# Kernel optimization log

Hardware: AMD Instinct MI355X
Metric: run time of the kernel (lower is better)

The kernel has to match this reference:

```python
import jax, jax.numpy as jnp
import numpy as np

DT = 0.05        # Euler step size
S_EULER = 2      # Euler steps between consecutive events, and after the last one (prop_to_end)


def setup_inputs() -> dict:
    key = jax.random.key(0)
    B, H, D, K, E = 512, 512, 128, 64, 256
    ks = jax.random.split(key, 16)

    def w(k, fan_in, fan_out):
        return jax.random.normal(k, (fan_in, fan_out), jnp.float32) / np.float32(np.sqrt(fan_in))

    X = jax.random.normal(ks[0], (K, E, D), jnp.float32)
    M = jax.random.bernoulli(ks[1], 0.5, (K, E, D)).astype(jnp.float32)
    # unique sample indices per event (irregular observation pattern, no scatter collisions)
    batch_idx = jax.vmap(lambda k: jax.random.permutation(k, B)[:E])(jax.random.split(ks[2], K))
    sample_idx = jnp.arange(B)
    b = lambda n: jnp.full((n,), 0.01, jnp.float32)  # torch init: bias filled with 0.01
    return {
        'X': X, 'M': M, 'batch_idx': batch_idx, 'sample_idx': sample_idx,
        'Wi': w(ks[3], D + H, H), 'bi': b(H),
        'Wf': w(ks[4], D + H, H), 'bf': b(H),
        'Wo': w(ks[5], D + H, H), 'bo': b(H),
        'Wc': w(ks[6], D + H, H), 'bc': b(H),
        'W1': w(ks[7], H, H), 'b1': b(H),
        'W2': w(ks[8], H, H), 'b2': b(H),
        'Wp1': w(ks[9], H, H), 'bp1': b(H),
        'Wp2': w(ks[10], H, D), 'bp2': b(D),
    }


def reference(X, M, batch_idx, sample_idx,
              Wi, bi, Wf, bf, Wo, bo, Wc, bc,
              W1, b1, W2, b2, Wp1, bp1, Wp2, bp2):
    B = sample_idx.shape[0]
    H = W1.shape[0]
    h0 = jnp.zeros((B, H), X.dtype)
    c0 = jnp.zeros((B, H), X.dtype)

    def euler(h):  # h <- h + dt * ODEFunc(h)
        return h + DT * (jnp.tanh(h @ W1 + b1) @ W2 + b2)

    def p_model(h):  # Linear -> ReLU -> (Dropout p=0, eval) -> Linear
        return jax.nn.relu(h @ Wp1 + bp1) @ Wp2 + bp2

    def step(carry, xs):
        h, c, loss, tot_m = carry
        Xo, Mo, idx = xs  # [E,D], [E,D], [E]
        for _ in range(S_EULER):
            h = euler(h)
        p = p_model(h)
        loss = loss + jnp.sum(jnp.abs(Xo - p[idx]) * Mo)
        tot_m = tot_m + jnp.sum(Mo)
        inp = jnp.concatenate([Xo, h[idx]], axis=-1)  # [E, D+H]
        ig = jax.nn.sigmoid(inp @ Wi + bi)
        fg = jax.nn.sigmoid(inp @ Wf + bf)
        og = jax.nn.sigmoid(inp @ Wo + bo)
        ct = jnp.tanh(inp @ Wc + bc)
        c_new = fg * c[idx] + ig * ct
        h_new = og * jnp.tanh(c_new)
        return (h.at[idx].set(h_new), c.at[idx].set(c_new), loss, tot_m), None

    init = (h0, c0, jnp.float32(0.0), jnp.float32(0.0))
    (h, c, loss, tot_m), _ = jax.lax.scan(step, init, (X, M, batch_idx))
    for _ in range(S_EULER):  # prop_to_end up to T
        h = euler(h)
    return jnp.stack([loss, loss / tot_m])
```

## Files before the change

### kernel.cpp

```cpp
#include <hip/hip_runtime.h>
#include <hip/hip_fp16.h>
#include <stdint.h>

#define Kn 64
#define En 256
#define Bn 512
#define Hn 512
#define Dn 128
#define NBLK 256
#define NTH  256
#define DT_C 0.05f


typedef _Float16 f16x8 __attribute__((ext_vector_type(8)));
typedef float    f32x4 __attribute__((ext_vector_type(4)));
typedef unsigned long long u64;

__device__ __forceinline__ float sigm(float x){ return 1.0f/(1.0f + __expf(-x)); }

__device__ __forceinline__ u64 ald(const u64* p){
  return __hip_atomic_load(p, __ATOMIC_RELAXED, __HIP_MEMORY_SCOPE_AGENT);
}
__device__ __forceinline__ void ast(u64* p, u64 v){
  __hip_atomic_store(p, v, __ATOMIC_RELAXED, __HIP_MEMORY_SCOPE_AGENT);
}

union HU { __half h[8]; u64 q[2]; uint32_t w[4]; };

__global__ void k_init(int* __restrict__ pos, float* __restrict__ acc,
                       int* __restrict__ ctr, uint32_t* __restrict__ hf){
  int i = blockIdx.x*blockDim.x + threadIdx.x;
  if (i < Kn*Bn) pos[i] = -1;
  if (i < 2) acc[i] = 0.0f;
  if (i < 1024) ctr[i] = 0;
  if (i < Hn*Hn/2) hf[i] = 0;
}

__global__ void k_scatter(const int* __restrict__ bidx, int* __restrict__ pos){
  int i = blockIdx.x*blockDim.x + threadIdx.x;
  if (i < Kn*En){
    int k = i >> 8;
    int e = i & (En-1);
    pos[(k << 9) | bidx[i]] = e;
  }
}

__global__ void k_cvt_frag(const float* __restrict__ src, __half* __restrict__ dst,
                           int KT, int N, int n){
  int i = blockIdx.x*blockDim.x + threadIdx.x;
  if (i >= n) return;
  int C = i / (KT*512);
  int r = i % (KT*512);
  int T = r >> 9;
  int q = r & 511;
  int l = q >> 3, e = q & 7;
  int srow = T*32 + ((l>>4)<<3) + e;
  int scol = C*16 + (l&15);
  dst[i] = __float2half(src[(size_t)srow*N + scol]);
}

__device__ __forceinline__ void gsync(int* c, int tgt){
  asm volatile("s_waitcnt vmcnt(0)" ::: "memory");
  __syncthreads();
  if (threadIdx.x == 0){
    __hip_atomic_fetch_add(c, 1, __ATOMIC_RELAXED, __HIP_MEMORY_SCOPE_AGENT);
    while (__hip_atomic_load(c, __ATOMIC_RELAXED, __HIP_MEMORY_SCOPE_AGENT) < tgt)
      __builtin_amdgcn_s_sleep(1);
  }
  __syncthreads();
}

__global__ __launch_bounds__(NTH, 1) void k_main(
  const float* __restrict__ X, const float* __restrict__ Mm,
  const int* __restrict__ pos, const __half* __restrict__ WF,
  __half* __restrict__ Hf, __half* __restrict__ Tf,
  const float* __restrict__ bi_, const float* __restrict__ bf_,
  const float* __restrict__ bo_, const float* __restrict__ bc_,
  const float* __restrict__ b1_, const float* __restrict__ b2_,
  const float* __restrict__ bp1_, const float* __restrict__ bp2_,
  float* __restrict__ acc, int* __restrict__ ctrbase)
{
  const __half* W1F  = WF;
  const __half* W2F  = WF + 262144;
  const __half* Wp1F = WF + 524288;
  const __half* Wp2F = WF + 786432;
  const __half* WgF  = WF + 851968;

  const int t    = threadIdx.x;
  const int bid  = blockIdx.x;
  const int s    = bid & 7;
  const int g    = bid >> 3;
  const int w    = t >> 6;
  const int lane = t & 63;

  int* ctr = ctrbase + g*32;

  __shared__ __align__(16) __half Afrag[16*512];
  __shared__ __align__(16) __half Xfrag[4*512];
  __shared__ __align__(16) float  outb[20*256];
  __shared__ float redbuf[8];

  const int row = t >> 4;
  const int q4  = t & 15;
  const int sc  = s*64 + q4*4;
  float Hreg[4] = {0,0,0,0};
  float Creg[4] = {0,0,0,0};
  float vb1[4], vb2[4], vbp1[4], vbi[4], vbf[4], vbo[4], vbc[4];
  #pragma unroll
  for (int i=0;i<4;i++){
    vb1[i]=b1_[sc+i]; vb2[i]=b2_[sc+i]; vbp1[i]=bp1_[sc+i];
    vbi[i]=bi_[sc+i]; vbf[i]=bf_[sc+i]; vbo[i]=bo_[sc+i]; vbc[i]=bc_[sc+i];
  }
  const float vbp2 = bp2_[s*16 + q4];

  f16x8 W1r[16], W2r[16], Wp1r[16];
  {
    const size_t cb = (size_t)(s*4 + w)*16*512 + lane*8;
    #pragma unroll
    for (int kt=0; kt<16; kt++){
      W1r[kt]  = *(const f16x8*)(W1F  + cb + kt*512);
      W2r[kt]  = *(const f16x8*)(W2F  + cb + kt*512);
      Wp1r[kt] = *(const f16x8*)(Wp1F + cb + kt*512);
    }
  }

  float loss_loc = 0.f, m_loc = 0.f;
  int round = 0;
  const int grow = g*16 + row;

  for (int k=0; k<Kn; k++){
    const int epos = pos[(k<<9) + grow];

    #pragma unroll 1
    for (int ph=0; ph<4; ph++){
      const __half* src = (ph & 1) ? Tf : Hf;
      {
        const int ar = t & 15, ch = t >> 4;
        const u64* sp = (const u64*)(src + ((size_t)(g*16+ar))*512 + ch*32);
        u64 v[8];
        #pragma unroll
        for (int i=0;i<8;i++) v[i] = ald(sp+i);
        #pragma unroll
        for (int kg=0;kg<4;kg++){
          u64* d = (u64*)(Afrag + ch*512 + (ar + 16*kg)*8);
          d[0] = v[2*kg]; d[1] = v[2*kg+1];
        }
      }
      __syncthreads();
      {
        f32x4 a4 = {0,0,0,0};
        if (!(ph & 1)){
          #pragma unroll
          for (int kt=0; kt<16; kt++){
            f16x8 a = *(const f16x8*)(Afrag + kt*512 + lane*8);
            a4 = __builtin_amdgcn_mfma_f32_16x16x32_f16(a, W1r[kt], a4, 0,0,0);
          }
        } else {
          #pragma unroll
          for (int kt=0; kt<16; kt++){
            f16x8 a = *(const f16x8*)(Afrag + kt*512 + lane*8);
            a4 = __builtin_amdgcn_mfma_f32_16x16x32_f16(a, W2r[kt], a4, 0,0,0);
          }
        }
        float* o = outb + w*256 + ((lane>>4)*4)*16 + (lane&15);
        o[0]=a4[0]; o[16]=a4[1]; o[32]=a4[2]; o[48]=a4[3];
      }
      __syncthreads();
      {
        const float* o = outb + (q4>>2)*256 + row*16 + (q4&3)*4;
        float v0=o[0], v1=o[1], v2=o[2], v3=o[3];
        HU u;
        if (!(ph & 1)){
          u.h[0]=__float2half(tanhf(v0+vb1[0])); u.h[1]=__float2half(tanhf(v1+vb1[1]));
          u.h[2]=__float2half(tanhf(v2+vb1[2])); u.h[3]=__float2half(tanhf(v3+vb1[3]));
          ast((u64*)(Tf + (size_t)grow*512 + sc), u.q[0]);
        } else {
          Hreg[0] += DT_C*(v0+vb2[0]); Hreg[1] += DT_C*(v1+vb2[1]);
          Hreg[2] += DT_C*(v2+vb2[2]); Hreg[3] += DT_C*(v3+vb2[3]);
          u.h[0]=__float2half(Hreg[0]); u.h[1]=__float2half(Hreg[1]);
          u.h[2]=__float2half(Hreg[2]); u.h[3]=__float2half(Hreg[3]);
          ast((u64*)(Hf + (size_t)grow*512 + sc), u.q[0]);
        }
      }
      gsync(ctr, 8*(++round));
    }

    {
      {
        const int ar = t & 15, ch = t >> 4;
        const u64* sp = (const u64*)(Hf + ((size_t)(g*16+ar))*512 + ch*32);
        u64 v[8];
        #pragma unroll
        for (int i=0;i<8;i++) v[i] = ald(sp+i);
        #pragma unroll
        for (int kg=0;kg<4;kg++){
          u64* d = (u64*)(Afrag + ch*512 + (ar + 16*kg)*8);
          d[0] = v[2*kg]; d[1] = v[2*kg+1];
        }
      }
      if (t < 64){
        const int ar = t & 15, ch = t >> 4;
        const int e = pos[(k<<9) + g*16 + ar];
        float xv[32];
        if (e >= 0){
          const float4* xp = (const float4*)(X + ((size_t)(k*En+e))*Dn + ch*32);
          #pragma unroll
          for (int i=0;i<8;i++){
            float4 f = xp[i];
            xv[4*i]=f.x; xv[4*i+1]=f.y; xv[4*i+2]=f.z; xv[4*i+3]=f.w;
          }
        } else {
          #pragma unroll
          for (int i=0;i<32;i++) xv[i]=0.f;
        }
        #pragma unroll
        for (int kg=0;kg<4;kg++){
          HU u;
          #pragma unroll
          for (int e8=0;e8<8;e8++) u.h[e8] = __float2half(xv[kg*8+e8]);
          u64* d = (u64*)(Xfrag + ch*512 + (ar + 16*kg)*8);
          d[0] = u.q[0]; d[1] = u.q[1];
        }
      }
      __syncthreads();
      {
        f32x4 a4 = {0,0,0,0};
        #pragma unroll
        for (int kt=0; kt<16; kt++){
          f16x8 a = *(const f16x8*)(Afrag + kt*512 + lane*8);
          a4 = __builtin_amdgcn_mfma_f32_16x16x32_f16(a, Wp1r[kt], a4, 0,0,0);
        }
        float* o = outb + (16+w)*256 + ((lane>>4)*4)*16 + (lane&15);
        o[0]=a4[0]; o[16]=a4[1]; o[32]=a4[2]; o[48]=a4[3];
      }
      #pragma unroll 1
      for (int i=0;i<4;i++){
        const int Cg = w*32 + s*4 + i;
        const __half* wb = WgF + (size_t)Cg*20*512;
        f32x4 a4 = {0,0,0,0};
        #pragma unroll 4
        for (int kt=0; kt<4; kt++){
          f16x8 a = *(const f16x8*)(Xfrag + kt*512 + lane*8);
          f16x8 b = *(const f16x8*)(wb + kt*512 + lane*8);
          a4 = __builtin_amdgcn_mfma_f32_16x16x32_f16(a, b, a4, 0,0,0);
        }
        #pragma unroll 4
        for (int kt=4; kt<20; kt++){
          f16x8 a = *(const f16x8*)(Afrag + (kt-4)*512 + lane*8);
          f16x8 b = *(const f16x8*)(wb + kt*512 + lane*8);
          a4 = __builtin_amdgcn_mfma_f32_16x16x32_f16(a, b, a4, 0,0,0);
        }
        float* o = outb + (w*4+i)*256 + ((lane>>4)*4)*16 + (lane&15);
        o[0]=a4[0]; o[16]=a4[1]; o[32]=a4[2]; o[48]=a4[3];
      }
      __syncthreads();
      {
        const float* o = outb + (16+(q4>>2))*256 + row*16 + (q4&3)*4;
        HU u;
        u.h[0]=__float2half(fmaxf(o[0]+vbp1[0],0.f));
        u.h[1]=__float2half(fmaxf(o[1]+vbp1[1],0.f));
        u.h[2]=__float2half(fmaxf(o[2]+vbp1[2],0.f));
        u.h[3]=__float2half(fmaxf(o[3]+vbp1[3],0.f));
        ast((u64*)(Tf + (size_t)grow*512 + sc), u.q[0]);
      }
      gsync(ctr, 8*(++round));
    }

    {
      {
        const int ar = t & 15, ch = t >> 4;
        const u64* sp = (const u64*)(Tf + ((size_t)(g*16+ar))*512 + ch*32);
        u64 v[8];
        #pragma unroll
        for (int i=0;i<8;i++) v[i] = ald(sp+i);
        #pragma unroll
        for (int kg=0;kg<4;kg++){
          u64* d = (u64*)(Afrag + ch*512 + (ar + 16*kg)*8);
          d[0] = v[2*kg]; d[1] = v[2*kg+1];
        }
      }
      __syncthreads();
      {
        const __half* wb = Wp2F + (size_t)s*16*512;
        f32x4 a4 = {0,0,0,0};
        #pragma unroll
        for (int kt2=0; kt2<4; kt2++){
          const int kt = w*4 + kt2;
          f16x8 a = *(const f16x8*)(Afrag + kt*512 + lane*8);
          f16x8 b = *(const f16x8*)(wb + kt*512 + lane*8);
          a4 = __builtin_amdgcn_mfma_f32_16x16x32_f16(a, b, a4, 0,0,0);
        }
        float* o = outb + (16+w)*256 + ((lane>>4)*4)*16 + (lane&15);
        o[0]=a4[0]; o[16]=a4[1]; o[32]=a4[2]; o[48]=a4[3];
      }
      if (epos >= 0){
        const int sub = q4 >> 2, off = row*16 + (q4&3)*4;
        const float4 pi = *(const float4*)(outb + (0*4+sub)*256 + off);
        const float4 pf = *(const float4*)(outb + (1*4+sub)*256 + off);
        const float4 po = *(const float4*)(outb + (2*4+sub)*256 + off);
        const float4 pc = *(const float4*)(outb + (3*4+sub)*256 + off);
        HU hu;
        const float gi[4]={pi.x,pi.y,pi.z,pi.w}, gf[4]={pf.x,pf.y,pf.z,pf.w};
        const float go[4]={po.x,po.y,po.z,po.w}, gc[4]={pc.x,pc.y,pc.z,pc.w};
        #pragma unroll
        for (int i=0;i<4;i++){
          float ig = sigm(gi[i] + vbi[i]);
          float fg = sigm(gf[i] + vbf[i]);
          float og = sigm(go[i] + vbo[i]);
          float ct = tanhf(gc[i] + vbc[i]);
          Creg[i] = fg*Creg[i] + ig*ct;
          Hreg[i] = og*tanhf(Creg[i]);
          hu.h[i] = __float2half(Hreg[i]);
        }
        ast((u64*)(Hf + (size_t)grow*512 + sc), hu.q[0]);
      }
      __syncthreads();
      if (epos >= 0){
        float p = outb[16*256 + row*16+q4] + outb[17*256 + row*16+q4]
                + outb[18*256 + row*16+q4] + outb[19*256 + row*16+q4] + vbp2;
        const int d = s*16 + q4;
        float xo = X[((size_t)(k*En+epos))*Dn + d];
        float mo = Mm[((size_t)(k*En+epos))*Dn + d];
        loss_loc += fabsf(xo - p)*mo;
        m_loc    += mo;
      }
      gsync(ctr, 8*(++round));
    }
  }

  #pragma unroll
  for (int off=32; off>0; off>>=1){
    loss_loc += __shfl_down(loss_loc, off);
    m_loc    += __shfl_down(m_loc, off);
  }
  if (lane == 0){ redbuf[w] = loss_loc; redbuf[4+w] = m_loc; }
  __syncthreads();
  if (t == 0){
    atomicAdd(acc+0, redbuf[0]+redbuf[1]+redbuf[2]+redbuf[3]);
    atomicAdd(acc+1, redbuf[4]+redbuf[5]+redbuf[6]+redbuf[7]);
  }
}

__global__ void k_fin(const float* __restrict__ acc, float* __restrict__ out){
  if (threadIdx.x == 0){
    out[0] = acc[0];
    out[1] = acc[0]/acc[1];
  }
}

extern "C" void kernel_launch(void* const* d_in, const int* in_sizes, int n_in,
                              void* d_out, int out_size, void* d_ws, size_t ws_size,
                              hipStream_t stream)
{
  const float* X   = (const float*)d_in[0];
  const float* Mm  = (const float*)d_in[1];
  const int*  bidx = (const int*)d_in[2];
  const float* Wi  = (const float*)d_in[4];
  const float* bi  = (const float*)d_in[5];
  const float* Wf  = (const float*)d_in[6];
  const float* bff = (const float*)d_in[7];
  const float* Wo  = (const float*)d_in[8];
  const float* bo  = (const float*)d_in[9];
  const float* Wc  = (const float*)d_in[10];
  const float* bc  = (const float*)d_in[11];
  const float* W1  = (const float*)d_in[12];
  const float* b1  = (const float*)d_in[13];
  const float* W2  = (const float*)d_in[14];
  const float* b2  = (const float*)d_in[15];
  const float* Wp1 = (const float*)d_in[16];
  const float* bp1 = (const float*)d_in[17];
  const float* Wp2 = (const float*)d_in[18];
  const float* bp2 = (const float*)d_in[19];

  char* ws = (char*)d_ws;
  int*    pos = (int*)ws;
  float*  acc = (float*)(ws + 131072);
  int*    ctr = (int*)(ws + 131200);
  __half* Hf  = (__half*)(ws + 1048576);
  __half* Tf  = (__half*)(ws + 1572864);
  __half* WF  = (__half*)(ws + 4194304);

  k_init   <<<512, 256, 0, stream>>>(pos, acc, ctr, (uint32_t*)Hf);
  k_scatter<<<(Kn*En + 255)/256, 256, 0, stream>>>(bidx, pos);

  k_cvt_frag<<<(262144+255)/256, 256, 0, stream>>>(W1,  WF,          16, 512, 262144);
  k_cvt_frag<<<(262144+255)/256, 256, 0, stream>>>(W2,  WF + 262144, 16, 512, 262144);
  k_cvt_frag<<<(262144+255)/256, 256, 0, stream>>>(Wp1, WF + 524288, 16, 512, 262144);
  k_cvt_frag<<<(65536 +255)/256, 256, 0, stream>>>(Wp2, WF + 786432, 16, 128, 65536);
  k_cvt_frag<<<(327680+255)/256, 256, 0, stream>>>(Wi,  WF + 851968,            20, 512, 327680);
  k_cvt_frag<<<(327680+255)/256, 256, 0, stream>>>(Wf,  WF + 851968 + 327680,   20, 512, 327680);
  k_cvt_frag<<<(327680+255)/256, 256, 0, stream>>>(Wo,  WF + 851968 + 655360,   20, 512, 327680);
  k_cvt_frag<<<(327680+255)/256, 256, 0, stream>>>(Wc,  WF + 851968 + 983040,   20, 512, 327680);

  k_main<<<NBLK, NTH, 0, stream>>>(X, Mm, pos, WF, Hf, Tf,
                                   bi, bff, bo, bc, b1, b2, bp1, bp2, acc, ctr);
  k_fin<<<1, 64, 0, stream>>>(acc, (float*)d_out);
}
```

Baseline: 1.916 ms.

## Replace counter barrier with per-block flags and defer Wp2 stage into next event

The shared atomic-counter group barrier becomes per-block round flags: each block publishes its own flag and polls the eight flags of its group, so the fetch-add read-modify-write is gone. The Wp2 projection and loss computation for event k are moved into the first Euler phase of event k+1, using separate buffers (T2f for the ReLU hidden state, Hf2 for the LSTM-updated h), which removes one grid-group sync per event. This cuts the syncs per event from six to five, at the cost of extra buffers, a selection between Hf and Hf2 per row, and an epilogue that handles the last event.

```diff
diff --git a/kernel.cpp b/kernel.cpp
--- a/kernel.cpp
+++ b/kernel.cpp
@@ -25,14 +25,14 @@
   __hip_atomic_store(p, v, __ATOMIC_RELAXED, __HIP_MEMORY_SCOPE_AGENT);
 }
 
-union HU { __half h[8]; u64 q[2]; uint32_t w[4]; };
+union HU { __half h[8]; u64 q[2]; };
 
 __global__ void k_init(int* __restrict__ pos, float* __restrict__ acc,
-                       int* __restrict__ ctr, uint32_t* __restrict__ hf){
+                       int* __restrict__ flg, uint32_t* __restrict__ hf){
   int i = blockIdx.x*blockDim.x + threadIdx.x;
   if (i < Kn*Bn) pos[i] = -1;
   if (i < 2) acc[i] = 0.0f;
-  if (i < 1024) ctr[i] = 0;
+  if (i < 32*8*32) flg[i] = 0;
   if (i < Hn*Hn/2) hf[i] = 0;
 }
 
@@ -59,26 +59,26 @@
   dst[i] = __float2half(src[(size_t)srow*N + scol]);
 }
 
-__device__ __forceinline__ void gsync(int* c, int tgt){
-  asm volatile("s_waitcnt vmcnt(0)" ::: "memory");
-  __syncthreads();
-  if (threadIdx.x == 0){
-    __hip_atomic_fetch_add(c, 1, __ATOMIC_RELAXED, __HIP_MEMORY_SCOPE_AGENT);
-    while (__hip_atomic_load(c, __ATOMIC_RELAXED, __HIP_MEMORY_SCOPE_AGENT) < tgt)
-      __builtin_amdgcn_s_sleep(1);
-  }
-  __syncthreads();
+__device__ __forceinline__ f32x4 mv16(const __half* Af, const f16x8* Wr, int lane){
+  f32x4 a = {0.f,0.f,0.f,0.f};
+  #pragma unroll
+  for (int kt=0; kt<16; kt++){
+    f16x8 av = *(const f16x8*)(Af + kt*512 + lane*8);
+    a = __builtin_amdgcn_mfma_f32_16x16x32_f16(av, Wr[kt], a, 0,0,0);
+  }
+  return a;
 }
 
 __global__ __launch_bounds__(NTH, 1) void k_main(
   const float* __restrict__ X, const float* __restrict__ Mm,
   const int* __restrict__ pos, const __half* __restrict__ WF,
   __half* __restrict__ Hf, __half* __restrict__ Tf,
+  __half* __restrict__ T2f, __half* __restrict__ Hf2,
   const float* __restrict__ bi_, const float* __restrict__ bf_,
   const float* __restrict__ bo_, const float* __restrict__ bc_,
   const float* __restrict__ b1_, const float* __restrict__ b2_,
   const float* __restrict__ bp1_, const float* __restrict__ bp2_,
-  float* __restrict__ acc, int* __restrict__ ctrbase)
+  float* __restrict__ acc, int* __restrict__ flg)
 {
   const __half* W1F  = WF;
   const __half* W2F  = WF + 262144;
@@ -92,10 +92,10 @@
   const int g    = bid >> 3;
   const int w    = t >> 6;
   const int lane = t & 63;
-
-  int* ctr = ctrbase + g*32;
+  int* flgbase = flg + g*8*32;
 
   __shared__ __align__(16) __half Afrag[16*512];
+  __shared__ __align__(16) __half Bfrag[16*512];
   __shared__ __align__(16) __half Xfrag[4*512];
   __shared__ __align__(16) float  outb[20*256];
   __shared__ float redbuf[8];
@@ -115,7 +115,7 @@
 
   f16x8 W1r[16], W2r[16], Wp1r[16];
   {
-    const size_t cb = (size_t)(s*4 + w)*16*512 + lane*8;
+    const size_t cb = (size_t)(s*4 + w)*16*512 + (size_t)lane*8;
     #pragma unroll
     for (int kt=0; kt<16; kt++){
       W1r[kt]  = *(const f16x8*)(W1F  + cb + kt*512);
@@ -125,206 +125,268 @@
   }
 
   float loss_loc = 0.f, m_loc = 0.f;
-  int round = 0;
+  int rnd = 0;
   const int grow = g*16 + row;
+
+#define POLL() do{                                                         \
+    if (t < 8){                                                            \
+      while (__hip_atomic_load(flgbase + t*32, __ATOMIC_RELAXED,           \
+                               __HIP_MEMORY_SCOPE_AGENT) < rnd)            \
+        __builtin_amdgcn_s_sleep(1);                                       \
+    }                                                                      \
+    __syncthreads();                                                       \
+  }while(0)
+
+#define PUBLISH() do{                                                      \
+    asm volatile("s_waitcnt vmcnt(0)" ::: "memory");                       \
+    __syncthreads();                                                       \
+    rnd++;                                                                 \
+    if (t == 0)                                                            \
+      __hip_atomic_store(flgbase + s*32, rnd, __ATOMIC_RELAXED,            \
+                         __HIP_MEMORY_SCOPE_AGENT);                        \
+  }while(0)
+
+#define STAGE(DST, SRCPTR) do{                                             \
+    const int ar = t & 15, ch = t >> 4;                                    \
+    const u64* sp = (const u64*)((SRCPTR) + ((size_t)(g*16+ar))*512 + ch*32); \
+    u64 v[8];                                                              \
+    _Pragma("unroll") for (int i=0;i<8;i++) v[i] = ald(sp+i);              \
+    _Pragma("unroll")                                                      \
+    for (int kg=0;kg<4;kg++){                                              \
+      u64* d = (u64*)((DST) + ch*512 + (ar + 16*kg)*8);                    \
+      d[0] = v[2*kg]; d[1] = v[2*kg+1];                                    \
+    }                                                                      \
+  }while(0)
 
   for (int k=0; k<Kn; k++){
     const int epos = pos[(k<<9) + grow];
 
-    #pragma unroll 1
-    for (int ph=0; ph<4; ph++){
-      const __half* src = (ph & 1) ? Tf : Hf;
-      {
-        const int ar = t & 15, ch = t >> 4;
-        const u64* sp = (const u64*)(src + ((size_t)(g*16+ar))*512 + ch*32);
-        u64 v[8];
-        #pragma unroll
-        for (int i=0;i<8;i++) v[i] = ald(sp+i);
-        #pragma unroll
-        for (int kg=0;kg<4;kg++){
-          u64* d = (u64*)(Afrag + ch*512 + (ar + 16*kg)*8);
-          d[0] = v[2*kg]; d[1] = v[2*kg+1];
-        }
-      }
-      __syncthreads();
-      {
-        f32x4 a4 = {0,0,0,0};
-        if (!(ph & 1)){
-          #pragma unroll
-          for (int kt=0; kt<16; kt++){
-            f16x8 a = *(const f16x8*)(Afrag + kt*512 + lane*8);
-            a4 = __builtin_amdgcn_mfma_f32_16x16x32_f16(a, W1r[kt], a4, 0,0,0);
-          }
-        } else {
-          #pragma unroll
-          for (int kt=0; kt<16; kt++){
-            f16x8 a = *(const f16x8*)(Afrag + kt*512 + lane*8);
-            a4 = __builtin_amdgcn_mfma_f32_16x16x32_f16(a, W2r[kt], a4, 0,0,0);
-          }
-        }
-        float* o = outb + w*256 + ((lane>>4)*4)*16 + (lane&15);
-        o[0]=a4[0]; o[16]=a4[1]; o[32]=a4[2]; o[48]=a4[3];
-      }
-      __syncthreads();
-      {
-        const float* o = outb + (q4>>2)*256 + row*16 + (q4&3)*4;
-        float v0=o[0], v1=o[1], v2=o[2], v3=o[3];
-        HU u;
-        if (!(ph & 1)){
-          u.h[0]=__float2half(tanhf(v0+vb1[0])); u.h[1]=__float2half(tanhf(v1+vb1[1]));
-          u.h[2]=__float2half(tanhf(v2+vb1[2])); u.h[3]=__float2half(tanhf(v3+vb1[3]));
-          ast((u64*)(Tf + (size_t)grow*512 + sc), u.q[0]);
-        } else {
-          Hreg[0] += DT_C*(v0+vb2[0]); Hreg[1] += DT_C*(v1+vb2[1]);
-          Hreg[2] += DT_C*(v2+vb2[2]); Hreg[3] += DT_C*(v3+vb2[3]);
-          u.h[0]=__float2half(Hreg[0]); u.h[1]=__float2half(Hreg[1]);
-          u.h[2]=__float2half(Hreg[2]); u.h[3]=__float2half(Hreg[3]);
-          ast((u64*)(Hf + (size_t)grow*512 + sc), u.q[0]);
-        }
-      }
-      gsync(ctr, 8*(++round));
-    }
-
-    {
-      {
-        const int ar = t & 15, ch = t >> 4;
-        const u64* sp = (const u64*)(Hf + ((size_t)(g*16+ar))*512 + ch*32);
-        u64 v[8];
-        #pragma unroll
-        for (int i=0;i<8;i++) v[i] = ald(sp+i);
-        #pragma unroll
-        for (int kg=0;kg<4;kg++){
-          u64* d = (u64*)(Afrag + ch*512 + (ar + 16*kg)*8);
-          d[0] = v[2*kg]; d[1] = v[2*kg+1];
-        }
-      }
-      if (t < 64){
-        const int ar = t & 15, ch = t >> 4;
-        const int e = pos[(k<<9) + g*16 + ar];
-        float xv[32];
-        if (e >= 0){
-          const float4* xp = (const float4*)(X + ((size_t)(k*En+e))*Dn + ch*32);
-          #pragma unroll
-          for (int i=0;i<8;i++){
-            float4 f = xp[i];
-            xv[4*i]=f.x; xv[4*i+1]=f.y; xv[4*i+2]=f.z; xv[4*i+3]=f.w;
-          }
-        } else {
-          #pragma unroll
-          for (int i=0;i<32;i++) xv[i]=0.f;
-        }
-        #pragma unroll
-        for (int kg=0;kg<4;kg++){
-          HU u;
-          #pragma unroll
-          for (int e8=0;e8<8;e8++) u.h[e8] = __float2half(xv[kg*8+e8]);
-          u64* d = (u64*)(Xfrag + ch*512 + (ar + 16*kg)*8);
-          d[0] = u.q[0]; d[1] = u.q[1];
-        }
-      }
-      __syncthreads();
-      {
-        f32x4 a4 = {0,0,0,0};
-        #pragma unroll
-        for (int kt=0; kt<16; kt++){
-          f16x8 a = *(const f16x8*)(Afrag + kt*512 + lane*8);
-          a4 = __builtin_amdgcn_mfma_f32_16x16x32_f16(a, Wp1r[kt], a4, 0,0,0);
-        }
-        float* o = outb + (16+w)*256 + ((lane>>4)*4)*16 + (lane&15);
-        o[0]=a4[0]; o[16]=a4[1]; o[32]=a4[2]; o[48]=a4[3];
-      }
-      #pragma unroll 1
-      for (int i=0;i<4;i++){
-        const int Cg = w*32 + s*4 + i;
-        const __half* wb = WgF + (size_t)Cg*20*512;
-        f32x4 a4 = {0,0,0,0};
-        #pragma unroll 4
-        for (int kt=0; kt<4; kt++){
-          f16x8 a = *(const f16x8*)(Xfrag + kt*512 + lane*8);
-          f16x8 b = *(const f16x8*)(wb + kt*512 + lane*8);
-          a4 = __builtin_amdgcn_mfma_f32_16x16x32_f16(a, b, a4, 0,0,0);
-        }
-        #pragma unroll 4
-        for (int kt=4; kt<20; kt++){
-          f16x8 a = *(const f16x8*)(Afrag + (kt-4)*512 + lane*8);
-          f16x8 b = *(const f16x8*)(wb + kt*512 + lane*8);
-          a4 = __builtin_amdgcn_mfma_f32_16x16x32_f16(a, b, a4, 0,0,0);
-        }
-        float* o = outb + (w*4+i)*256 + ((lane>>4)*4)*16 + (lane&15);
-        o[0]=a4[0]; o[16]=a4[1]; o[32]=a4[2]; o[48]=a4[3];
-      }
-      __syncthreads();
-      {
-        const float* o = outb + (16+(q4>>2))*256 + row*16 + (q4&3)*4;
-        HU u;
-        u.h[0]=__float2half(fmaxf(o[0]+vbp1[0],0.f));
-        u.h[1]=__float2half(fmaxf(o[1]+vbp1[1],0.f));
-        u.h[2]=__float2half(fmaxf(o[2]+vbp1[2],0.f));
-        u.h[3]=__float2half(fmaxf(o[3]+vbp1[3],0.f));
-        ast((u64*)(Tf + (size_t)grow*512 + sc), u.q[0]);
-      }
-      gsync(ctr, 8*(++round));
-    }
-
-    {
-      {
-        const int ar = t & 15, ch = t >> 4;
-        const u64* sp = (const u64*)(Tf + ((size_t)(g*16+ar))*512 + ch*32);
-        u64 v[8];
-        #pragma unroll
-        for (int i=0;i<8;i++) v[i] = ald(sp+i);
-        #pragma unroll
-        for (int kg=0;kg<4;kg++){
-          u64* d = (u64*)(Afrag + ch*512 + (ar + 16*kg)*8);
-          d[0] = v[2*kg]; d[1] = v[2*kg+1];
-        }
-      }
-      __syncthreads();
-      {
-        const __half* wb = Wp2F + (size_t)s*16*512;
-        f32x4 a4 = {0,0,0,0};
-        #pragma unroll
-        for (int kt2=0; kt2<4; kt2++){
-          const int kt = w*4 + kt2;
-          f16x8 a = *(const f16x8*)(Afrag + kt*512 + lane*8);
-          f16x8 b = *(const f16x8*)(wb + kt*512 + lane*8);
-          a4 = __builtin_amdgcn_mfma_f32_16x16x32_f16(a, b, a4, 0,0,0);
-        }
-        float* o = outb + (16+w)*256 + ((lane>>4)*4)*16 + (lane&15);
-        o[0]=a4[0]; o[16]=a4[1]; o[32]=a4[2]; o[48]=a4[3];
-      }
-      if (epos >= 0){
-        const int sub = q4 >> 2, off = row*16 + (q4&3)*4;
-        const float4 pi = *(const float4*)(outb + (0*4+sub)*256 + off);
-        const float4 pf = *(const float4*)(outb + (1*4+sub)*256 + off);
-        const float4 po = *(const float4*)(outb + (2*4+sub)*256 + off);
-        const float4 pc = *(const float4*)(outb + (3*4+sub)*256 + off);
-        HU hu;
-        const float gi[4]={pi.x,pi.y,pi.z,pi.w}, gf[4]={pf.x,pf.y,pf.z,pf.w};
-        const float go[4]={po.x,po.y,po.z,po.w}, gc[4]={pc.x,pc.y,pc.z,pc.w};
-        #pragma unroll
-        for (int i=0;i<4;i++){
-          float ig = sigm(gi[i] + vbi[i]);
-          float fg = sigm(gf[i] + vbf[i]);
-          float og = sigm(go[i] + vbo[i]);
-          float ct = tanhf(gc[i] + vbc[i]);
-          Creg[i] = fg*Creg[i] + ig*ct;
-          Hreg[i] = og*tanhf(Creg[i]);
-          hu.h[i] = __float2half(Hreg[i]);
-        }
-        ast((u64*)(Hf + (size_t)grow*512 + sc), hu.q[0]);
-      }
-      __syncthreads();
-      if (epos >= 0){
+    POLL();
+    if (k > 0) STAGE(Bfrag, T2f);
+    {
+      const int ar = t & 15, ch = t >> 4;
+      const __half* hsrc = Hf;
+      if (k > 0 && pos[((k-1)<<9) + g*16 + ar] >= 0) hsrc = Hf2;
+      const u64* sp = (const u64*)(hsrc + ((size_t)(g*16+ar))*512 + ch*32);
+      u64 v[8];
+      #pragma unroll
+      for (int i=0;i<8;i++) v[i] = ald(sp+i);
+      #pragma unroll
+      for (int kg=0;kg<4;kg++){
+        u64* d = (u64*)(Afrag + ch*512 + (ar + 16*kg)*8);
+        d[0] = v[2*kg]; d[1] = v[2*kg+1];
+      }
+    }
+    __syncthreads();
+    {
+      f32x4 a4 = mv16(Afrag, W1r, lane);
+      float* o = outb + w*256 + ((lane>>4)*4)*16 + (lane&15);
+      o[0]=a4[0]; o[16]=a4[1]; o[32]=a4[2]; o[48]=a4[3];
+    }
+    if (k > 0){
+      const __half* wb = Wp2F + (size_t)s*16*512;
+      f32x4 a4 = {0,0,0,0};
+      #pragma unroll
+      for (int kt2=0; kt2<4; kt2++){
+        const int kt = w*4 + kt2;
+        f16x8 a = *(const f16x8*)(Bfrag + kt*512 + lane*8);
+        f16x8 b = *(const f16x8*)(wb + kt*512 + lane*8);
+        a4 = __builtin_amdgcn_mfma_f32_16x16x32_f16(a, b, a4, 0,0,0);
+      }
+      float* o = outb + (16+w)*256 + ((lane>>4)*4)*16 + (lane&15);
+      o[0]=a4[0]; o[16]=a4[1]; o[32]=a4[2]; o[48]=a4[3];
+    }
+    __syncthreads();
+    {
+      const float* o = outb + (q4>>2)*256 + row*16 + (q4&3)*4;
+      HU u;
+      u.h[0]=__float2half(tanhf(o[0]+vb1[0])); u.h[1]=__float2half(tanhf(o[1]+vb1[1]));
+      u.h[2]=__float2half(tanhf(o[2]+vb1[2])); u.h[3]=__float2half(tanhf(o[3]+vb1[3]));
+      ast((u64*)(Tf + (size_t)grow*512 + sc), u.q[0]);
+    }
+    PUBLISH();
+    if (k > 0){
+      const int ep = pos[((k-1)<<9) + g*16 + row];
+      if (ep >= 0){
         float p = outb[16*256 + row*16+q4] + outb[17*256 + row*16+q4]
                 + outb[18*256 + row*16+q4] + outb[19*256 + row*16+q4] + vbp2;
-        const int d = s*16 + q4;
-        float xo = X[((size_t)(k*En+epos))*Dn + d];
-        float mo = Mm[((size_t)(k*En+epos))*Dn + d];
-        loss_loc += fabsf(xo - p)*mo;
+        const size_t xo = ((size_t)((k-1)*En+ep))*Dn + s*16 + q4;
+        float mo = Mm[xo];
+        loss_loc += fabsf(X[xo] - p)*mo;
         m_loc    += mo;
       }
-      gsync(ctr, 8*(++round));
+    }
+
+    POLL();
+    STAGE(Afrag, Tf);
+    __syncthreads();
+    {
+      f32x4 a4 = mv16(Afrag, W2r, lane);
+      float* o = outb + w*256 + ((lane>>4)*4)*16 + (lane&15);
+      o[0]=a4[0]; o[16]=a4[1]; o[32]=a4[2]; o[48]=a4[3];
+    }
+    __syncthreads();
+    {
+      const float* o = outb + (q4>>2)*256 + row*16 + (q4&3)*4;
+      HU u;
+      Hreg[0] += DT_C*(o[0]+vb2[0]); Hreg[1] += DT_C*(o[1]+vb2[1]);
+      Hreg[2] += DT_C*(o[2]+vb2[2]); Hreg[3] += DT_C*(o[3]+vb2[3]);
+      u.h[0]=__float2half(Hreg[0]); u.h[1]=__float2half(Hreg[1]);
+      u.h[2]=__float2half(Hreg[2]); u.h[3]=__float2half(Hreg[3]);
+      ast((u64*)(Hf + (size_t)grow*512 + sc), u.q[0]);
+    }
+    PUBLISH();
+
+    POLL();
+    STAGE(Afrag, Hf);
+    __syncthreads();
+    {
+      f32x4 a4 = mv16(Afrag, W1r, lane);
+      float* o = outb + w*256 + ((lane>>4)*4)*16 + (lane&15);
+      o[0]=a4[0]; o[16]=a4[1]; o[32]=a4[2]; o[48]=a4[3];
+    }
+    __syncthreads();
+    {
+      const float* o = outb + (q4>>2)*256 + row*16 + (q4&3)*4;
+      HU u;
+      u.h[0]=__float2half(tanhf(o[0]+vb1[0])); u.h[1]=__float2half(tanhf(o[1]+vb1[1]));
+      u.h[2]=__float2half(tanhf(o[2]+vb1[2])); u.h[3]=__float2half(tanhf(o[3]+vb1[3]));
+      ast((u64*)(Tf + (size_t)grow*512 + sc), u.q[0]);
+    }
+    PUBLISH();
+
+    POLL();
+    STAGE(Afrag, Tf);
+    __syncthreads();
+    {
+      f32x4 a4 = mv16(Afrag, W2r, lane);
+      float* o = outb + w*256 + ((lane>>4)*4)*16 + (lane&15);
+      o[0]=a4[0]; o[16]=a4[1]; o[32]=a4[2]; o[48]=a4[3];
+    }
+    __syncthreads();
+    {
+      const float* o = outb + (q4>>2)*256 + row*16 + (q4&3)*4;
+      HU u;
+      Hreg[0] += DT_C*(o[0]+vb2[0]); Hreg[1] += DT_C*(o[1]+vb2[1]);
+      Hreg[2] += DT_C*(o[2]+vb2[2]); Hreg[3] += DT_C*(o[3]+vb2[3]);
+      u.h[0]=__float2half(Hreg[0]); u.h[1]=__float2half(Hreg[1]);
+      u.h[2]=__float2half(Hreg[2]); u.h[3]=__float2half(Hreg[3]);
+      ast((u64*)(Hf + (size_t)grow*512 + sc), u.q[0]);
+    }
+    PUBLISH();
+
+    POLL();
+    STAGE(Afrag, Hf);
+    if (t < 64){
+      const int ar = t & 15, ch = t >> 4;
+      const int e = pos[(k<<9) + g*16 + ar];
+      float xv[32];
+      if (e >= 0){
+        const float4* xp = (const float4*)(X + ((size_t)(k*En+e))*Dn + ch*32);
+        #pragma unroll
+        for (int i=0;i<8;i++){
+          float4 f = xp[i];
+          xv[4*i]=f.x; xv[4*i+1]=f.y; xv[4*i+2]=f.z; xv[4*i+3]=f.w;
+        }
+      } else {
+        #pragma unroll
+        for (int i=0;i<32;i++) xv[i]=0.f;
+      }
+      #pragma unroll
+      for (int kg=0;kg<4;kg++){
+        HU u;
+        #pragma unroll
+        for (int e8=0;e8<8;e8++) u.h[e8] = __float2half(xv[kg*8+e8]);
+        u64* d = (u64*)(Xfrag + ch*512 + (ar + 16*kg)*8);
+        d[0] = u.q[0]; d[1] = u.q[1];
+      }
+    }
+    __syncthreads();
+    {
+      f32x4 a4 = mv16(Afrag, Wp1r, lane);
+      float* o = outb + (16+w)*256 + ((lane>>4)*4)*16 + (lane&15);
+      o[0]=a4[0]; o[16]=a4[1]; o[32]=a4[2]; o[48]=a4[3];
+    }
+    #pragma unroll 1
+    for (int i=0;i<4;i++){
+      const int Cg = w*32 + s*4 + i;
+      const __half* wb = WgF + (size_t)Cg*20*512;
+      f32x4 a4 = {0,0,0,0};
+      #pragma unroll 4
+      for (int kt=0; kt<4; kt++){
+        f16x8 a = *(const f16x8*)(Xfrag + kt*512 + lane*8);
+        f16x8 b = *(const f16x8*)(wb + kt*512 + lane*8);
+        a4 = __builtin_amdgcn_mfma_f32_16x16x32_f16(a, b, a4, 0,0,0);
+      }
+      #pragma unroll 4
+      for (int kt=4; kt<20; kt++){
+        f16x8 a = *(const f16x8*)(Afrag + (kt-4)*512 + lane*8);
+        f16x8 b = *(const f16x8*)(wb + kt*512 + lane*8);
+        a4 = __builtin_amdgcn_mfma_f32_16x16x32_f16(a, b, a4, 0,0,0);
+      }
+      float* o = outb + (w*4+i)*256 + ((lane>>4)*4)*16 + (lane&15);
+      o[0]=a4[0]; o[16]=a4[1]; o[32]=a4[2]; o[48]=a4[3];
+    }
+    __syncthreads();
+    {
+      const float* o = outb + (16+(q4>>2))*256 + row*16 + (q4&3)*4;
+      HU u;
+      u.h[0]=__float2half(fmaxf(o[0]+vbp1[0],0.f));
+      u.h[1]=__float2half(fmaxf(o[1]+vbp1[1],0.f));
+      u.h[2]=__float2half(fmaxf(o[2]+vbp1[2],0.f));
+      u.h[3]=__float2half(fmaxf(o[3]+vbp1[3],0.f));
+      ast((u64*)(T2f + (size_t)grow*512 + sc), u.q[0]);
+    }
+    if (epos >= 0){
+      const int sub = q4 >> 2, off = row*16 + (q4&3)*4;
+      const float4 pi = *(const float4*)(outb + (0*4+sub)*256 + off);
+      const float4 pf = *(const float4*)(outb + (1*4+sub)*256 + off);
+      const float4 po = *(const float4*)(outb + (2*4+sub)*256 + off);
+      const float4 pc = *(const float4*)(outb + (3*4+sub)*256 + off);
+      HU hu;
+      const float gi[4]={pi.x,pi.y,pi.z,pi.w}, gf[4]={pf.x,pf.y,pf.z,pf.w};
+      const float go[4]={po.x,po.y,po.z,po.w}, gc[4]={pc.x,pc.y,pc.z,pc.w};
+      #pragma unroll
+      for (int i=0;i<4;i++){
+        float ig = sigm(gi[i] + vbi[i]);
+        float fg = sigm(gf[i] + vbf[i]);
+        float og = sigm(go[i] + vbo[i]);
+        float ct = tanhf(gc[i] + vbc[i]);
+        Creg[i] = fg*Creg[i] + ig*ct;
+        Hreg[i] = og*tanhf(Creg[i]);
+        hu.h[i] = __float2half(Hreg[i]);
+      }
+      ast((u64*)(Hf2 + (size_t)grow*512 + sc), hu.q[0]);
+    }
+    PUBLISH();
+  }
+
+  POLL();
+  STAGE(Bfrag, T2f);
+  __syncthreads();
+  {
+    const __half* wb = Wp2F + (size_t)s*16*512;
+    f32x4 a4 = {0,0,0,0};
+    #pragma unroll
+    for (int kt2=0; kt2<4; kt2++){
+      const int kt = w*4 + kt2;
+      f16x8 a = *(const f16x8*)(Bfrag + kt*512 + lane*8);
+      f16x8 b = *(const f16x8*)(wb + kt*512 + lane*8);
+      a4 = __builtin_amdgcn_mfma_f32_16x16x32_f16(a, b, a4, 0,0,0);
+    }
+    float* o = outb + (16+w)*256 + ((lane>>4)*4)*16 + (lane&15);
+    o[0]=a4[0]; o[16]=a4[1]; o[32]=a4[2]; o[48]=a4[3];
+  }
+  __syncthreads();
+  {
+    const int ep = pos[((Kn-1)<<9) + g*16 + row];
+    if (ep >= 0){
+      float p = outb[16*256 + row*16+q4] + outb[17*256 + row*16+q4]
+              + outb[18*256 + row*16+q4] + outb[19*256 + row*16+q4] + vbp2;
+      const size_t xo = ((size_t)((Kn-1)*En+ep))*Dn + s*16 + q4;
+      float mo = Mm[xo];
+      loss_loc += fabsf(X[xo] - p)*mo;
+      m_loc    += mo;
     }
   }
 
@@ -339,6 +401,9 @@
     atomicAdd(acc+0, redbuf[0]+redbuf[1]+redbuf[2]+redbuf[3]);
     atomicAdd(acc+1, redbuf[4]+redbuf[5]+redbuf[6]+redbuf[7]);
   }
+#undef POLL
+#undef PUBLISH
+#undef STAGE
 }
 
 __global__ void k_fin(const float* __restrict__ acc, float* __restrict__ out){
@@ -375,12 +440,14 @@
   char* ws = (char*)d_ws;
   int*    pos = (int*)ws;
   float*  acc = (float*)(ws + 131072);
-  int*    ctr = (int*)(ws + 131200);
+  int*    flg = (int*)(ws + 196608);
   __half* Hf  = (__half*)(ws + 1048576);
   __half* Tf  = (__half*)(ws + 1572864);
+  __half* T2f = (__half*)(ws + 2097152);
+  __half* Hf2 = (__half*)(ws + 2621440);
   __half* WF  = (__half*)(ws + 4194304);
 
-  k_init   <<<512, 256, 0, stream>>>(pos, acc, ctr, (uint32_t*)Hf);
+  k_init   <<<512, 256, 0, stream>>>(pos, acc, flg, (uint32_t*)Hf);
   k_scatter<<<(Kn*En + 255)/256, 256, 0, stream>>>(bidx, pos);
 
   k_cvt_frag<<<(262144+255)/256, 256, 0, stream>>>(W1,  WF,          16, 512, 262144);
@@ -392,7 +459,7 @@
   k_cvt_frag<<<(327680+255)/256, 256, 0, stream>>>(Wo,  WF + 851968 + 655360,   20, 512, 327680);
   k_cvt_frag<<<(327680+255)/256, 256, 0, stream>>>(Wc,  WF + 851968 + 983040,   20, 512, 327680);
 
-  k_main<<<NBLK, NTH, 0, stream>>>(X, Mm, pos, WF, Hf, Tf,
-                                   bi, bff, bo, bc, b1, b2, bp1, bp2, acc, ctr);
+  k_main<<<NBLK, NTH, 0, stream>>>(X, Mm, pos, WF, Hf, Tf, T2f, Hf2,
+                                   bi, bff, bo, bc, b1, b2, bp1, bp2, acc, flg);
   k_fin<<<1, 64, 0, stream>>>(acc, (float*)d_out);
 }
```

Result: no change. 1.893 ms, median of 3 (-1.2%).
